# Kernel optimization log

Hardware: AMD Instinct MI355X
Metric: run time of the kernel (lower is better)

The kernel has to match this reference:

```python
import jax, jax.numpy as jnp
import numpy as np

N = 50000      # num nodes
E = 400000     # num edges
B = 64         # num graphs
D_IN = 768
DIMS = [512, 256, 128]
CH = 64        # classifier hidden
NC = 2         # num classes
EPS = 1e-5


def setup_inputs() -> dict:
    key = jax.random.key(0)
    ks = jax.random.split(key, 12)
    inp = {}
    inp["x"] = jax.random.normal(ks[0], (N, D_IN), jnp.float32)
    inp["edge_index"] = jax.random.randint(ks[1], (2, E), 0, N, dtype=jnp.int32)
    inp["batch"] = jnp.sort(jax.random.randint(ks[2], (N,), 0, B, dtype=jnp.int32))
    dims = [D_IN] + DIMS
    for i in range(3):
        inp[f"W{i}"] = jax.random.normal(ks[3 + i], (dims[i], dims[i + 1]), jnp.float32) / np.sqrt(dims[i]).astype(np.float32)
        inp[f"b{i}"] = jnp.zeros((dims[i + 1],), jnp.float32)
        inp[f"gamma{i}"] = jnp.ones((dims[i + 1],), jnp.float32)
        inp[f"beta{i}"] = jnp.zeros((dims[i + 1],), jnp.float32)
    inp["Wc1"] = jax.random.normal(ks[6], (2 * DIMS[-1], CH), jnp.float32) / np.sqrt(2 * DIMS[-1]).astype(np.float32)
    inp["bc1"] = jnp.zeros((CH,), jnp.float32)
    inp["gamma_c"] = jnp.ones((CH,), jnp.float32)
    inp["beta_c"] = jnp.zeros((CH,), jnp.float32)
    inp["Wc2"] = jax.random.normal(ks[7], (CH, NC), jnp.float32) / np.sqrt(CH).astype(np.float32)
    inp["bc2"] = jnp.zeros((NC,), jnp.float32)
    return inp


def _batchnorm(h, gamma, beta):
    # training-mode BatchNorm1d: biased batch statistics over the node axis
    m = jnp.mean(h, axis=0)
    v = jnp.var(h, axis=0)
    return (h - m) * jax.lax.rsqrt(v + EPS) * gamma + beta


def _forward(x, edge_index, batch, params):
    # GCN normalization with self-loops: norm_e = deg[src]^-1/2 * deg[dst]^-1/2
    loops = jnp.arange(N, dtype=edge_index.dtype)
    src = jnp.concatenate([edge_index[0], loops])
    dst = jnp.concatenate([edge_index[1], loops])
    deg = jax.ops.segment_sum(jnp.ones_like(dst, jnp.float32), dst, num_segments=N)
    dis = jax.lax.rsqrt(deg)  # deg >= 1 due to self loops
    norm = dis[src] * dis[dst]  # [E+N]

    n_layers = len(params)
    h = x
    for i, (W, b, g, be) in enumerate(params):
        hw = h @ W                                   # [N, out_dim]
        msg = hw[src] * norm[:, None]                # gather + scale, [E+N, out_dim]
        h = jax.ops.segment_sum(msg, dst, num_segments=N) + b
        h = _batchnorm(h, g, be)
        if i < n_layers - 1:
            h = jax.nn.relu(h)
        # dropout: identity in eval; residual never fires (dims 512/256 != 128)
    return h


def reference(x, edge_index, batch,
              W0, b0, gamma0, beta0,
              W1, b1, gamma1, beta1,
              W2, b2, gamma2, beta2,
              Wc1, bc1, gamma_c, beta_c, Wc2, bc2):
    params = [(W0, b0, gamma0, beta0), (W1, b1, gamma1, beta1), (W2, b2, gamma2, beta2)]
    h = _forward(x, edge_index, batch, params)       # [N, 128]

    # mean_max global pooling over graphs
    ones = jnp.ones((N,), jnp.float32)
    cnt = jnp.maximum(jax.ops.segment_sum(ones, batch, num_segments=B), 1.0)
    mean_pool = jax.ops.segment_sum(h, batch, num_segments=B) / cnt[:, None]
    max_pool = jax.ops.segment_max(h, batch, num_segments=B)
    g = jnp.concatenate([mean_pool, max_pool], axis=1)  # [B, 256]

    # classifier: Linear -> ReLU -> BatchNorm -> (Dropout=id) -> Linear
    hc = jax.nn.relu(g @ Wc1 + bc1)
    hc = _batchnorm(hc, gamma_c, beta_c)
    logits = hc @ Wc2 + bc2                          # [B, 2]
    return logits
```

## Files before the change

### kernel.cpp

```cpp
#include <hip/hip_runtime.h>
#include <cstddef>

#define NN 50000
#define EE 400000
#define BB 64
#define MP 50048
#define BN_EPS 1e-5f
#define PSEG 32

typedef __attribute__((ext_vector_type(8))) short s16x8;
typedef __attribute__((ext_vector_type(4))) float f32x4;
typedef __attribute__((ext_vector_type(8))) _Float16 f16x8;

#define GLOAD_LDS16(g, l) __builtin_amdgcn_global_load_lds( \
    (const __attribute__((address_space(1))) void*)(g),     \
    (__attribute__((address_space(3))) void*)(l), 16, 0, 0)

__global__ void fill_f32(float* __restrict__ p, int n, float v) {
    int i = blockIdx.x * blockDim.x + threadIdx.x;
    if (i < n) p[i] = v;
}

__global__ void fill_i32(int* __restrict__ p, int n, int v) {
    int i = blockIdx.x * blockDim.x + threadIdx.x;
    if (i < n) p[i] = v;
}

__global__ void deg_edges(const int* __restrict__ ei, int* __restrict__ deg) {
    int e = blockIdx.x * blockDim.x + threadIdx.x;
    if (e < EE) atomicAdd(&deg[ei[EE + e]], 1);
}

__global__ void cvt_wt_planes(const float* __restrict__ W,
                              unsigned short* __restrict__ Wh,
                              unsigned short* __restrict__ Wl,
                              int K, int N) {
    int i = blockIdx.x * blockDim.x + threadIdx.x;
    if (i >= K * N) return;
    int k = i / N, n = i % N;
    float f = W[i];
    unsigned int fb = __float_as_uint(f);
    unsigned int hif = fb & 0xFFFF0000u;
    float lo = f - __uint_as_float(hif);
    Wh[(size_t)n * K + k] = (unsigned short)(hif >> 16);
    Wl[(size_t)n * K + k] = (unsigned short)(__float_as_uint(lo) >> 16);
}

__global__ __launch_bounds__(256) void scan_block(const int* __restrict__ deg,
                                                  int* __restrict__ rowptr,
                                                  int* __restrict__ bsum,
                                                  float* __restrict__ dis) {
    __shared__ int tmp[256];
    int tid = threadIdx.x;
    int i = blockIdx.x * 256 + tid;
    int v = (i < NN) ? deg[i] : 0;
    if (i < NN) dis[i] = rsqrtf((float)v + 1.0f);
    tmp[tid] = v;
    __syncthreads();
#pragma unroll
    for (int off = 1; off < 256; off <<= 1) {
        int t = (tid >= off) ? tmp[tid - off] : 0;
        __syncthreads();
        tmp[tid] += t;
        __syncthreads();
    }
    if (i < NN) rowptr[i] = tmp[tid] - v;
    if (tid == 255) bsum[blockIdx.x] = tmp[255];
}

__global__ __launch_bounds__(256) void scan_sums(const int* __restrict__ bsum,
                                                 int* __restrict__ boff, int nb) {
    __shared__ int tmp[256];
    int tid = threadIdx.x;
    int v = (tid < nb) ? bsum[tid] : 0;
    tmp[tid] = v;
    __syncthreads();
#pragma unroll
    for (int off = 1; off < 256; off <<= 1) {
        int t = (tid >= off) ? tmp[tid - off] : 0;
        __syncthreads();
        tmp[tid] += t;
        __syncthreads();
    }
    boff[tid] = tmp[tid] - v;
}

__global__ void scan_fixup(int* __restrict__ rowptr, const int* __restrict__ boff,
                           int* __restrict__ cursor) {
    int i = blockIdx.x * blockDim.x + threadIdx.x;
    if (i < NN) {
        int v = rowptr[i] + boff[i >> 8];
        rowptr[i] = v;
        cursor[i] = v;
    }
    if (i == 0) rowptr[NN] = EE;
}

__global__ void fill_csr(const int* __restrict__ ei, int* __restrict__ cursor,
                         int* __restrict__ csr_src) {
    int e = blockIdx.x * blockDim.x + threadIdx.x;
    if (e >= EE) return;
    int s = ei[e];
    int t = ei[EE + e];
    int pos = atomicAdd(&cursor[t], 1);
    csr_src[pos] = s;
}

static __device__ __forceinline__ void split8(const float* __restrict__ f,
                                              s16x8& h, s16x8& l) {
    unsigned int hi[8], lo[8];
#pragma unroll
    for (int j = 0; j < 8; ++j) {
        unsigned int e = __float_as_uint(f[j]);
        hi[j] = e & 0xFFFF0000u;
        float lf = f[j] - __uint_as_float(hi[j]);
        lo[j] = __float_as_uint(lf);
    }
    union { s16x8 v; unsigned int u[4]; } H, L;
#pragma unroll
    for (int k = 0; k < 4; ++k) {
        H.u[k] = (hi[2 * k + 1]) | (hi[2 * k] >> 16);
        L.u[k] = (lo[2 * k + 1] & 0xFFFF0000u) | (lo[2 * k] >> 16);
    }
    h = H.v; l = L.v;
}

template <int AMODE>
__global__ __launch_bounds__(256) void gemm_split3(const unsigned int* __restrict__ A,
                                                   const unsigned short* __restrict__ Bh,
                                                   const unsigned short* __restrict__ Bl,
                                                   _Float16* __restrict__ C,
                                                   const float* __restrict__ dis,
                                                   const float* __restrict__ c1p,
                                                   const float* __restrict__ c2p,
                                                   int K, int N) {
    __shared__ unsigned int As[2][128 * 32];
    __shared__ unsigned short Bsh[2][128 * 32];
    __shared__ unsigned short Bsl[2][128 * 32];
    const int tid = threadIdx.x;
    const int w  = tid >> 6;
    const int lw = tid & 63;
    const int lo = lw & 15;
    const int hi = lw >> 4;
    const int wr = w >> 1, wc = w & 1;

    const int nwg = gridDim.x;
    const int q = nwg >> 3, r = nwg & 7;
    int orig = blockIdx.x;
    int xcd = orig & 7, idx = orig >> 3;
    int lid = (xcd < r) ? (xcd * (q + 1) + idx) : (r * (q + 1) + (xcd - r) * q + idx);
    const int nbx = N >> 7;
    const int lbx = (nbx == 4) ? 2 : (nbx == 2 ? 1 : 0);
    const int rowBase = (lid >> lbx) * 128;
    const int colBase = (lid & (nbx - 1)) * 128;

    const int arow = w * 8 + (lw >> 3);
    const int acol = ((lw & 7) ^ (lw >> 3)) * 4;
    const int brow = w * 16 + (lw >> 2);
    const int bcol = ((lw & 3) ^ ((lw >> 2) & 3)) * 8;

    f32x4 acc[4][4];
#pragma unroll
    for (int m = 0; m < 4; ++m)
#pragma unroll
        for (int n = 0; n < 4; ++n) acc[m][n] = (f32x4){0.f, 0.f, 0.f, 0.f};

#define STAGE(buf, k0s) do {                                                        \
    _Pragma("unroll")                                                               \
    for (int i_ = 0; i_ < 4; ++i_) {                                                \
        int gr_ = rowBase + i_ * 32 + arow;                                         \
        gr_ = (gr_ < NN) ? gr_ : (NN - 1);                                          \
        GLOAD_LDS16(A + (size_t)gr_ * K + (k0s) + acol,                             \
                    (char*)&As[buf][0] + i_ * 4096 + w * 1024);                     \
    }                                                                               \
    _Pragma("unroll")                                                               \
    for (int j_ = 0; j_ < 2; ++j_) {                                                \
        int gc_ = colBase + j_ * 64 + brow;                                         \
        GLOAD_LDS16(Bh + (size_t)gc_ * K + (k0s) + bcol,                            \
                    (char*)&Bsh[buf][0] + j_ * 4096 + w * 1024);                    \
        GLOAD_LDS16(Bl + (size_t)gc_ * K + (k0s) + bcol,                            \
                    (char*)&Bsl[buf][0] + j_ * 4096 + w * 1024);                    \
    }                                                                               \
} while (0)

    STAGE(0, 0);
    asm volatile("s_waitcnt vmcnt(0)" ::: "memory");
    __builtin_amdgcn_s_barrier();

    const int nt = K >> 5;
    int cur = 0;
    for (int t = 0; t < nt; ++t) {
        if (t + 1 < nt) STAGE(cur ^ 1, (t + 1) << 5);

        float c1v[8], c2v[8];
        if (AMODE == 2) {
            int kb = (t << 5) + hi * 8;
            f32x4 a0 = *(const f32x4*)&c1p[kb];
            f32x4 a1 = *(const f32x4*)&c1p[kb + 4];
            f32x4 b0 = *(const f32x4*)&c2p[kb];
            f32x4 b1 = *(const f32x4*)&c2p[kb + 4];
#pragma unroll
            for (int j = 0; j < 4; ++j) {
                c1v[j] = a0[j]; c1v[4 + j] = a1[j];
                c2v[j] = b0[j]; c2v[4 + j] = b1[j];
            }
        }

        s16x8 ah[4], al[4], bh[4], bl[4];
#pragma unroll
        for (int m = 0; m < 4; ++m) {
            int rr = wr * 64 + m * 16 + lo;
            int c0 = ((hi * 2) ^ (rr & 7)) * 4;
            int c1 = ((hi * 2 + 1) ^ (rr & 7)) * 4;
            uint4 u0 = *(const uint4*)&As[cur][rr * 32 + c0];
            uint4 u1 = *(const uint4*)&As[cur][rr * 32 + c1];
            float f[8];
            f[0] = __uint_as_float(u0.x); f[1] = __uint_as_float(u0.y);
            f[2] = __uint_as_float(u0.z); f[3] = __uint_as_float(u0.w);
            f[4] = __uint_as_float(u1.x); f[5] = __uint_as_float(u1.y);
            f[6] = __uint_as_float(u1.z); f[7] = __uint_as_float(u1.w);
            if (AMODE == 2) {
#pragma unroll
                for (int j = 0; j < 8; ++j)
                    f[j] = fmaxf(f[j] * c1v[j] + c2v[j], 0.f);
            }
            split8(f, ah[m], al[m]);
        }
#pragma unroll
        for (int n = 0; n < 4; ++n) {
            int rr = wc * 64 + n * 16 + lo;
            int cb = (hi ^ (rr & 3)) * 8;
            bh[n] = *(const s16x8*)&Bsh[cur][rr * 32 + cb];
            bl[n] = *(const s16x8*)&Bsl[cur][rr * 32 + cb];
        }
#pragma unroll
        for (int m = 0; m < 4; ++m)
#pragma unroll
            for (int n = 0; n < 4; ++n) {
                acc[m][n] = __builtin_amdgcn_mfma_f32_16x16x32_bf16(ah[m], bh[n], acc[m][n], 0, 0, 0);
                acc[m][n] = __builtin_amdgcn_mfma_f32_16x16x32_bf16(ah[m], bl[n], acc[m][n], 0, 0, 0);
                acc[m][n] = __builtin_amdgcn_mfma_f32_16x16x32_bf16(al[m], bh[n], acc[m][n], 0, 0, 0);
            }

        asm volatile("s_waitcnt vmcnt(0)" ::: "memory");
        __builtin_amdgcn_s_barrier();
        cur ^= 1;
    }
#undef STAGE

#pragma unroll
    for (int m = 0; m < 4; ++m) {
        int row0 = rowBase + wr * 64 + m * 16 + hi * 4;
#pragma unroll
        for (int j = 0; j < 4; ++j) {
            int rr = row0 + j;
            float ds = dis[(rr < NN) ? rr : (NN - 1)];
#pragma unroll
            for (int n = 0; n < 4; ++n) {
                int col = colBase + wc * 64 + n * 16 + lo;
                C[(size_t)rr * N + col] = (_Float16)(ds * acc[m][n][j]);
            }
        }
    }
}

__global__ __launch_bounds__(256) void agg_gather(const _Float16* __restrict__ hws,
                                                  float* __restrict__ agg,
                                                  const int* __restrict__ rowptr,
                                                  const int* __restrict__ csr_src,
                                                  const float* __restrict__ dis,
                                                  const float* __restrict__ bias,
                                                  int D) {
    const int tpn = D >> 3;
    const int npb = 256 / tpn;
    const int local = threadIdx.x / tpn;
    const int lane = threadIdx.x % tpn;
    const int n = blockIdx.x * npb + local;
    if (n >= NN) return;
    const int dq = lane * 8;

    f16x8 sv = *(const f16x8*)&hws[(size_t)n * D + dq];
    float a[8];
#pragma unroll
    for (int j = 0; j < 8; ++j) a[j] = (float)sv[j];

    int e0 = rowptr[n], e1 = rowptr[n + 1];
    int e = e0;
    for (; e + 4 <= e1; e += 4) {
        int s0 = csr_src[e + 0];
        int s1 = csr_src[e + 1];
        int s2 = csr_src[e + 2];
        int s3 = csr_src[e + 3];
        f16x8 v0 = *(const f16x8*)&hws[(size_t)s0 * D + dq];
        f16x8 v1 = *(const f16x8*)&hws[(size_t)s1 * D + dq];
        f16x8 v2 = *(const f16x8*)&hws[(size_t)s2 * D + dq];
        f16x8 v3 = *(const f16x8*)&hws[(size_t)s3 * D + dq];
#pragma unroll
        for (int j = 0; j < 8; ++j)
            a[j] += ((float)v0[j] + (float)v1[j]) + ((float)v2[j] + (float)v3[j]);
    }
    for (; e < e1; ++e) {
        int s = csr_src[e];
        f16x8 v = *(const f16x8*)&hws[(size_t)s * D + dq];
#pragma unroll
        for (int j = 0; j < 8; ++j) a[j] += (float)v[j];
    }

    float din = dis[n];
    f32x4 o0, o1;
#pragma unroll
    for (int j = 0; j < 4; ++j) o0[j] = din * a[j] + bias[dq + j];
#pragma unroll
    for (int j = 0; j < 4; ++j) o1[j] = din * a[4 + j] + bias[dq + 4 + j];
    *(f32x4*)&agg[(size_t)n * D + dq] = o0;
    *(f32x4*)&agg[(size_t)n * D + dq + 4] = o1;
}

__global__ void bn_stats(const float* __restrict__ h, float* __restrict__ stats, int D) {
    int d = blockIdx.x * blockDim.x + threadIdx.x;
    if (d >= D) return;
    float s = 0.f, ss = 0.f;
    for (int n = blockIdx.y; n < NN; n += gridDim.y) {
        float v = h[(size_t)n * D + d];
        s += v;
        ss += v * v;
    }
    atomicAdd(&stats[d], s);
    atomicAdd(&stats[D + d], ss);
}

__global__ void bn_coef(const float* __restrict__ stats,
                        const float* __restrict__ gamma, const float* __restrict__ beta,
                        float* __restrict__ c1, float* __restrict__ c2, int D) {
    int d = blockIdx.x * blockDim.x + threadIdx.x;
    if (d >= D) return;
    float mean = stats[d] * (1.0f / NN);
    float var  = stats[D + d] * (1.0f / NN) - mean * mean;
    float r = rsqrtf(var + BN_EPS) * gamma[d];
    c1[d] = r;
    c2[d] = beta[d] - mean * r;
}

__global__ void find_starts(const int* __restrict__ batch, int* __restrict__ start) {
    int n = blockIdx.x * blockDim.x + threadIdx.x;
    if (n >= NN) return;
    int bc = batch[n];
    int bp = (n == 0) ? -1 : batch[n - 1];
    for (int g = bp + 1; g <= bc; ++g) start[g] = n;
    if (n == NN - 1) {
        for (int g = bc + 1; g <= BB; ++g) start[g] = NN;
    }
}

__global__ void pool_part(const float* __restrict__ h, const int* __restrict__ start,
                          const float* __restrict__ c1, const float* __restrict__ c2,
                          float* __restrict__ part) {
    int b = blockIdx.x;
    int seg = blockIdx.y;
    int d = threadIdx.x;
    int s0 = start[b], s1 = start[b + 1];
    int len = s1 - s0;
    int a = s0 + (int)((long long)len * seg / PSEG);
    int e = s0 + (int)((long long)len * (seg + 1) / PSEG);
    float a1 = c1[d], a2 = c2[d];
    float sum = 0.f;
    float mx = -3.402823466e+38f;
    for (int n = a; n < e; ++n) {
        float v = a1 * h[(size_t)n * 128 + d] + a2;
        sum += v;
        mx = fmaxf(mx, v);
    }
    part[(size_t)(b * PSEG + seg) * 256 + d] = sum;
    part[(size_t)(b * PSEG + seg) * 256 + 128 + d] = mx;
}

__global__ void pool_reduce(const float* __restrict__ part, const int* __restrict__ start,
                            float* __restrict__ pool) {
    int b = blockIdx.x;
    int d = threadIdx.x;
    float sum = 0.f;
    float mx = -3.402823466e+38f;
    for (int s = 0; s < PSEG; ++s) {
        sum += part[(size_t)(b * PSEG + s) * 256 + d];
        mx = fmaxf(mx, part[(size_t)(b * PSEG + s) * 256 + 128 + d]);
    }
    float cnt = fmaxf((float)(start[b + 1] - start[b]), 1.0f);
    pool[b * 256 + d] = sum / cnt;
    pool[b * 256 + 128 + d] = mx;
}

__global__ __launch_bounds__(256) void classifier_kernel(
        const float* __restrict__ pool,
        const float* __restrict__ Wc1, const float* __restrict__ bc1,
        const float* __restrict__ gc, const float* __restrict__ bec,
        const float* __restrict__ Wc2, const float* __restrict__ bc2,
        float* __restrict__ out) {
    __shared__ float hc[64][65];
    __shared__ float cmean[64];
    __shared__ float crstd[64];
    int tid = threadIdx.x;

    for (int i = tid; i < 64 * 64; i += 256) {
        int r = i / 64, c = i % 64;
        float acc = bc1[c];
        for (int k = 0; k < 256; ++k)
            acc += pool[r * 256 + k] * Wc1[k * 64 + c];
        hc[r][c] = fmaxf(acc, 0.f);
    }
    __syncthreads();

    if (tid < 64) {
        float s = 0.f, ss = 0.f;
        for (int r = 0; r < 64; ++r) {
            float v = hc[r][tid];
            s += v;
            ss += v * v;
        }
        float m = s * (1.0f / 64.0f);
        float var = ss * (1.0f / 64.0f) - m * m;
        cmean[tid] = m;
        crstd[tid] = rsqrtf(var + BN_EPS);
    }
    __syncthreads();

    if (tid < 128) {
        int r = tid / 2, k = tid % 2;
        float acc = bc2[k];
        for (int c = 0; c < 64; ++c) {
            float v = (hc[r][c] - cmean[c]) * crstd[c] * gc[c] + bec[c];
            acc += v * Wc2[c * 2 + k];
        }
        out[r * 2 + k] = acc;
    }
}

extern "C" void kernel_launch(void* const* d_in, const int* in_sizes, int n_in,
                              void* d_out, int out_size, void* d_ws, size_t ws_size,
                              hipStream_t stream) {
    const float* x     = (const float*)d_in[0];
    const int*   ei    = (const int*)d_in[1];
    const int*   batch = (const int*)d_in[2];
    const float* W[3]  = {(const float*)d_in[3], (const float*)d_in[7], (const float*)d_in[11]};
    const float* bbv[3] = {(const float*)d_in[4], (const float*)d_in[8], (const float*)d_in[12]};
    const float* gm[3] = {(const float*)d_in[5], (const float*)d_in[9], (const float*)d_in[13]};
    const float* bt[3] = {(const float*)d_in[6], (const float*)d_in[10], (const float*)d_in[14]};
    const float* Wc1 = (const float*)d_in[15];
    const float* bc1 = (const float*)d_in[16];
    const float* gc  = (const float*)d_in[17];
    const float* bec = (const float*)d_in[18];
    const float* Wc2 = (const float*)d_in[19];
    const float* bc2 = (const float*)d_in[20];
    float* out = (float*)d_out;

    char* p = (char*)d_ws;
    _Float16* hw = (_Float16*)p; p += (size_t)MP * 512 * 2;
    float* agg = (float*)p; p += (size_t)NN * 512 * 4;
    unsigned short* Wh[3];
    unsigned short* Wl[3];
    Wh[0] = (unsigned short*)p; p += (size_t)512 * 768 * 2;
    Wl[0] = (unsigned short*)p; p += (size_t)512 * 768 * 2;
    Wh[1] = (unsigned short*)p; p += (size_t)256 * 512 * 2;
    Wl[1] = (unsigned short*)p; p += (size_t)256 * 512 * 2;
    Wh[2] = (unsigned short*)p; p += (size_t)128 * 256 * 2;
    Wl[2] = (unsigned short*)p; p += (size_t)128 * 256 * 2;
    float* dis   = (float*)p; p += (size_t)NN * 4;
    float* stats = (float*)p; p += 1024 * 4;
    float* c1v   = (float*)p; p += 512 * 4;
    float* c2v   = (float*)p; p += 512 * 4;
    float* pool  = (float*)p; p += (size_t)BB * 256 * 4;
    float* part  = (float*)p; p += (size_t)BB * PSEG * 256 * 4;
    int* deg_i   = (int*)p; p += (size_t)NN * 4;
    int* rowptr  = (int*)p; p += (size_t)(NN + 1) * 4;
    int* cursor  = (int*)p; p += (size_t)NN * 4;
    int* bsum    = (int*)p; p += 256 * 4;
    int* boff    = (int*)p; p += 256 * 4;
    int* csr_src = (int*)p; p += (size_t)EE * 4;
    int* start   = (int*)p; p += (BB + 1) * 4;

    const int nb = (NN + 255) / 256;

    cvt_wt_planes<<<(768 * 512 + 255) / 256, 256, 0, stream>>>(W[0], Wh[0], Wl[0], 768, 512);
    cvt_wt_planes<<<(512 * 256 + 255) / 256, 256, 0, stream>>>(W[1], Wh[1], Wl[1], 512, 256);
    cvt_wt_planes<<<(256 * 128 + 255) / 256, 256, 0, stream>>>(W[2], Wh[2], Wl[2], 256, 128);

    fill_i32<<<nb, 256, 0, stream>>>(deg_i, NN, 0);
    deg_edges<<<(EE + 255) / 256, 256, 0, stream>>>(ei, deg_i);
    scan_block<<<nb, 256, 0, stream>>>(deg_i, rowptr, bsum, dis);
    scan_sums<<<1, 256, 0, stream>>>(bsum, boff, nb);
    scan_fixup<<<nb, 256, 0, stream>>>(rowptr, boff, cursor);
    fill_csr<<<(EE + 255) / 256, 256, 0, stream>>>(ei, cursor, csr_src);

    const int dims[4] = {768, 512, 256, 128};

    for (int l = 0; l < 3; ++l) {
        int K = dims[l], D = dims[l + 1];

        int nwg = (D / 128) * (MP / 128);
        if (l == 0)
            gemm_split3<0><<<nwg, 256, 0, stream>>>((const unsigned int*)x, Wh[0], Wl[0],
                                                    hw, dis, nullptr, nullptr, K, D);
        else
            gemm_split3<2><<<nwg, 256, 0, stream>>>((const unsigned int*)agg, Wh[l], Wl[l],
                                                    hw, dis, c1v, c2v, K, D);

        int tpn = D / 8;
        int npb = 256 / tpn;
        agg_gather<<<(NN + npb - 1) / npb, 256, 0, stream>>>(hw, agg, rowptr, csr_src,
                                                             dis, bbv[l], D);

        fill_f32<<<(2 * D + 255) / 256, 256, 0, stream>>>(stats, 2 * D, 0.0f);
        bn_stats<<<dim3((D + 255) / 256, 256), 256, 0, stream>>>(agg, stats, D);
        bn_coef<<<1, D, 0, stream>>>(stats, gm[l], bt[l], c1v, c2v, D);
    }

    find_starts<<<nb, 256, 0, stream>>>(batch, start);
    dim3 pg(BB, PSEG);
    pool_part<<<pg, 128, 0, stream>>>(agg, start, c1v, c2v, part);
    pool_reduce<<<BB, 128, 0, stream>>>(part, start, pool);
    classifier_kernel<<<1, 256, 0, stream>>>(pool, Wc1, bc1, gc, bec, Wc2, bc2, out);
}
```

Baseline: 741.2 us.

## Replace double-buffered LDS staging in split-bf16 GEMM with single buffer

Removes the ping-pong LDS buffers and the prefetch of the next K tile in the split3 GEMM. Each iteration now loads its tile, synchronizes, computes, and synchronizes again. This halves LDS use per workgroup, which may allow more resident workgroups per CU, but global-load latency is no longer overlapped with MFMA work inside a block. Correctness relies on __syncthreads draining the global_load_lds operations before the LDS reads.

```diff
diff --git a/kernel.cpp b/kernel.cpp
--- a/kernel.cpp
+++ b/kernel.cpp
@@ -134,9 +134,9 @@
                                                    const float* __restrict__ c1p,
                                                    const float* __restrict__ c2p,
                                                    int K, int N) {
-    __shared__ unsigned int As[2][128 * 32];
-    __shared__ unsigned short Bsh[2][128 * 32];
-    __shared__ unsigned short Bsl[2][128 * 32];
+    __shared__ unsigned int As[128 * 32];
+    __shared__ unsigned short Bsh[128 * 32];
+    __shared__ unsigned short Bsl[128 * 32];
     const int tid = threadIdx.x;
     const int w  = tid >> 6;
     const int lw = tid & 63;
@@ -165,36 +165,26 @@
 #pragma unroll
         for (int n = 0; n < 4; ++n) acc[m][n] = (f32x4){0.f, 0.f, 0.f, 0.f};
 
-#define STAGE(buf, k0s) do {                                                        \
-    _Pragma("unroll")                                                               \
-    for (int i_ = 0; i_ < 4; ++i_) {                                                \
-        int gr_ = rowBase + i_ * 32 + arow;                                         \
-        gr_ = (gr_ < NN) ? gr_ : (NN - 1);                                          \
-        GLOAD_LDS16(A + (size_t)gr_ * K + (k0s) + acol,                             \
-                    (char*)&As[buf][0] + i_ * 4096 + w * 1024);                     \
-    }                                                                               \
-    _Pragma("unroll")                                                               \
-    for (int j_ = 0; j_ < 2; ++j_) {                                                \
-        int gc_ = colBase + j_ * 64 + brow;                                         \
-        GLOAD_LDS16(Bh + (size_t)gc_ * K + (k0s) + bcol,                            \
-                    (char*)&Bsh[buf][0] + j_ * 4096 + w * 1024);                    \
-        GLOAD_LDS16(Bl + (size_t)gc_ * K + (k0s) + bcol,                            \
-                    (char*)&Bsl[buf][0] + j_ * 4096 + w * 1024);                    \
-    }                                                                               \
-} while (0)
-
-    STAGE(0, 0);
-    asm volatile("s_waitcnt vmcnt(0)" ::: "memory");
-    __builtin_amdgcn_s_barrier();
-
     const int nt = K >> 5;
-    int cur = 0;
     for (int t = 0; t < nt; ++t) {
-        if (t + 1 < nt) STAGE(cur ^ 1, (t + 1) << 5);
+        const int k0s = t << 5;
+#pragma unroll
+        for (int i_ = 0; i_ < 4; ++i_) {
+            int gr_ = rowBase + i_ * 32 + arow;
+            gr_ = (gr_ < NN) ? gr_ : (NN - 1);
+            GLOAD_LDS16(A + (size_t)gr_ * K + k0s + acol, (char*)As + i_ * 4096 + w * 1024);
+        }
+#pragma unroll
+        for (int j_ = 0; j_ < 2; ++j_) {
+            int gc_ = colBase + j_ * 64 + brow;
+            GLOAD_LDS16(Bh + (size_t)gc_ * K + k0s + bcol, (char*)Bsh + j_ * 4096 + w * 1024);
+            GLOAD_LDS16(Bl + (size_t)gc_ * K + k0s + bcol, (char*)Bsl + j_ * 4096 + w * 1024);
+        }
+        __syncthreads();
 
         float c1v[8], c2v[8];
         if (AMODE == 2) {
-            int kb = (t << 5) + hi * 8;
+            int kb = k0s + hi * 8;
             f32x4 a0 = *(const f32x4*)&c1p[kb];
             f32x4 a1 = *(const f32x4*)&c1p[kb + 4];
             f32x4 b0 = *(const f32x4*)&c2p[kb];
@@ -212,8 +202,8 @@
             int rr = wr * 64 + m * 16 + lo;
             int c0 = ((hi * 2) ^ (rr & 7)) * 4;
             int c1 = ((hi * 2 + 1) ^ (rr & 7)) * 4;
-            uint4 u0 = *(const uint4*)&As[cur][rr * 32 + c0];
-            uint4 u1 = *(const uint4*)&As[cur][rr * 32 + c1];
+            uint4 u0 = *(const uint4*)&As[rr * 32 + c0];
+            uint4 u1 = *(const uint4*)&As[rr * 32 + c1];
             float f[8];
             f[0] = __uint_as_float(u0.x); f[1] = __uint_as_float(u0.y);
             f[2] = __uint_as_float(u0.z); f[3] = __uint_as_float(u0.w);
@@ -230,8 +220,8 @@
         for (int n = 0; n < 4; ++n) {
             int rr = wc * 64 + n * 16 + lo;
             int cb = (hi ^ (rr & 3)) * 8;
-            bh[n] = *(const s16x8*)&Bsh[cur][rr * 32 + cb];
-            bl[n] = *(const s16x8*)&Bsl[cur][rr * 32 + cb];
+            bh[n] = *(const s16x8*)&Bsh[rr * 32 + cb];
+            bl[n] = *(const s16x8*)&Bsl[rr * 32 + cb];
         }
 #pragma unroll
         for (int m = 0; m < 4; ++m)
@@ -241,12 +231,8 @@
                 acc[m][n] = __builtin_amdgcn_mfma_f32_16x16x32_bf16(ah[m], bl[n], acc[m][n], 0, 0, 0);
                 acc[m][n] = __builtin_amdgcn_mfma_f32_16x16x32_bf16(al[m], bh[n], acc[m][n], 0, 0, 0);
             }
-
-        asm volatile("s_waitcnt vmcnt(0)" ::: "memory");
-        __builtin_amdgcn_s_barrier();
-        cur ^= 1;
-    }
-#undef STAGE
+        __syncthreads();
+    }
 
 #pragma unroll
     for (int m = 0; m < 4; ++m) {
```

New measurement: 762.4 us. 2.9% more time.
